# Kernel optimization log

Hardware: AMD Instinct MI355X
Metric: run time of the kernel (lower is better)

## Reference

```python
import jax, jax.numpy as jnp
import numpy as np

B, T, N, K, HD = 4, 32, 1024, 16, 128
IN_CH = 4


def _knn_idx(q, r, k):
    # q, r: [..., 3, N]. dist(n, m) = ||q[..., n] - r[..., m]||
    # expanded-norm form avoids materializing [..., 3, N, N]
    q2 = jnp.sum(q * q, axis=-2)                     # [..., N]
    r2 = jnp.sum(r * r, axis=-2)                     # [..., N]
    qr = jnp.einsum('...cn,...cm->...nm', q, r)      # [..., N, N]
    d2 = q2[..., :, None] + r2[..., None, :] - 2.0 * qr
    _, idx = jax.lax.top_k(-d2, k)                   # smallest-k (sqrt is monotone)
    return idx                                       # [..., N, K]


def _gather_nbrs(feat, idx):
    # feat [B, C, N], idx [B, N, K] -> [B, C, N, K]; out[b,c,n,k] = feat[b,c,idx[b,n,k]]
    return jax.vmap(lambda f, i: f[:, i])(feat, idx)


def _lstm_layer(cur_in, position, pos_past, group_ind, w, b, hd):
    # cur_in [B,T,C,N]; position/pos_past [B,T,4,N]; group_ind [B,T,N,K]
    Bb, Tt, C, Nn = cur_in.shape
    h0 = jnp.zeros((Bb, hd, Nn), cur_in.dtype)
    c0 = jnp.zeros_like(h0)

    def step(carry, inp):
        h, c = carry                                  # [B,hd,N]
        xt, pp, idx = inp                             # [B,C,N], [B,4,N], [B,N,K]
        h_with_pos = jnp.concatenate([pp, h], axis=1) # [B,4+hd,N]
        hg = _gather_nbrs(h_with_pos, idx)            # [B,4+hd,N,K]
        cg = _gather_nbrs(c, idx)                     # [B,hd,N,K]
        # cell subtracts center position from first 4 channels of hidden
        hg = jnp.concatenate([hg[:, :4] - xt[:, :4, :, None], hg[:, 4:]], axis=1)
        xk = jnp.broadcast_to(xt[..., None], xt.shape + (idx.shape[-1],))
        comb = jnp.concatenate([xk, hg], axis=1)      # [B, C+4+hd, N, K]
        gates = jnp.einsum('bink,oi->bonk', comb, w) + b[None, :, None, None]
        ci, cf, co, cgt = jnp.split(gates, 4, axis=1)
        c_next = jax.nn.sigmoid(cf) * cg + jax.nn.sigmoid(ci) * jnp.tanh(cgt)
        h_next = jax.nn.sigmoid(co) * jnp.tanh(c_next)
        h_new = jnp.max(h_next, axis=-1)              # AdaptiveMaxPool2d((None,1)) over K
        c_new = jnp.max(c_next, axis=-1)
        return (h_new, c_new), h_new

    xs = (jnp.moveaxis(cur_in, 1, 0), jnp.moveaxis(pos_past, 1, 0),
          jnp.moveaxis(group_ind, 1, 0))
    (h, c), hs = jax.lax.scan(step, (h0, c0), xs)
    hs = jnp.moveaxis(hs, 0, 1)                       # [B,T,hd,N]
    layer_out = jnp.concatenate([position, hs], axis=2)  # [B,T,4+hd,N]
    return layer_out, h, c


def _forward(x, w0, b0, w1, b1):
    position = x[:, :, :4]                            # [B,T,4,N]
    p3 = position[:, :, :3]
    idx0 = _knn_idx(p3[:, 0], p3[:, 0], K)[:, None]   # [B,1,N,K] (frame 0 vs itself)
    idxr = _knn_idx(p3[:, 1:], p3[:, :-1], K)         # [B,T-1,N,K] (frame t vs t-1)
    group_ind = jnp.concatenate([idx0, idxr], axis=1)  # [B,T,N,K]
    # past-frame positions (t=0 uses frame 0)
    pos_past = jnp.concatenate([position[:, :1], position[:, :-1]], axis=1)
    out0, h, c = _lstm_layer(x,    position, pos_past, group_ind, w0, b0, HD)
    out1, h, c = _lstm_layer(out0, position, pos_past, group_ind, w1, b1, HD)
    return out1, h, c, group_ind


def setup_inputs() -> dict:
    key = jax.random.key(0)
    ks = jax.random.split(key, 3)
    x = jax.random.normal(ks[0], (B, T, IN_CH, N), jnp.float32)
    # 1x1 conv weights flattened to [out, in]; layer0 in=4+4+128=136, layer1 in=132+4+128=264
    w0 = jax.random.normal(ks[1], (4 * HD, IN_CH + 4 + HD), jnp.float32) * 0.05
    b0 = jnp.zeros((4 * HD,), jnp.float32)
    w1 = jax.random.normal(ks[2], (4 * HD, (HD + 4) + 4 + HD), jnp.float32) * 0.05
    b1 = jnp.zeros((4 * HD,), jnp.float32)
    return {"x": x, "w0": w0, "b0": b0, "w1": w1, "b1": b1}


def reference(x, w0, b0, w1, b1):
    out1, h, c, group_ind = _forward(x, w0, b0, w1, b1)
    # match torch shapes: trailing singleton dim
    return out1[..., None], h[..., None], c[..., None], group_ind
```

## Files before the change

kernel.cpp:

```cpp
#include <hip/hip_runtime.h>
#include <math.h>

#define BB 4
#define TT 32
#define NN 1024
#define KK 16
#define HDIM 128
#define NO 512
#define KG 132

#define OUT1_SZ ((size_t)BB*TT*132*NN)
#define OH (OUT1_SZ)
#define OC (OH + (size_t)BB*HDIM*NN)
#define OG (OC + (size_t)BB*HDIM*NN)

__global__ __launch_bounds__(256) void prep_weights(
    const float* __restrict__ w0, const float* __restrict__ w1,
    float* __restrict__ WaT0, float* __restrict__ WgT0,
    float* __restrict__ WaT1, float* __restrict__ WgT1)
{
  int idx = blockIdx.x * 256 + threadIdx.x;
  if (idx >= KG * NO) return;
  int k = idx / NO, o = idx - k * NO;
  WgT0[idx] = w0[o * 136 + 4 + k];
  WgT1[idx] = w1[o * 264 + 132 + k];
  float a1 = w1[o * 264 + k];
  if (k < 4) a1 -= w1[o * 264 + 132 + k];
  WaT1[idx] = a1;
  if (k < 4) WaT0[k * NO + o] = w0[o * 136 + k] - w0[o * 136 + 4 + k];
}

__global__ __launch_bounds__(512) void knn_kernel(
    const float* __restrict__ x, int* __restrict__ gind, float* __restrict__ gfloat)
{
  __shared__ float rx[NN], ry[NN], rz[NN], rr[NN];
  int b = blockIdx.z, t = blockIdx.y;
  int tp = (t == 0) ? 0 : t - 1;
  const float* xr = x + (size_t)(b * TT + tp) * 4 * NN;
  for (int m = threadIdx.x; m < NN; m += 512) {
    float a = xr[m], e = xr[NN + m], c = xr[2 * NN + m];
    rx[m] = a; ry[m] = e; rz[m] = c;
    rr[m] = __fadd_rn(__fadd_rn(__fmul_rn(a, a), __fmul_rn(e, e)), __fmul_rn(c, c));
  }
  __syncthreads();
  int n = blockIdx.x * 512 + threadIdx.x;
  const float* xq = x + (size_t)(b * TT + t) * 4 * NN;
  float qx = xq[n], qy = xq[NN + n], qz = xq[2 * NN + n];
  float q2 = __fadd_rn(__fadd_rn(__fmul_rn(qx, qx), __fmul_rn(qy, qy)), __fmul_rn(qz, qz));
  float bd[KK]; int bi[KK];
#pragma unroll
  for (int i = 0; i < KK; ++i) { bd[i] = 3.402823466e38f; bi[i] = 0; }
  for (int m = 0; m < NN; ++m) {
    float s = __fmaf_rn(qz, rz[m], __fmaf_rn(qy, ry[m], __fmaf_rn(qx, rx[m], 0.0f)));
    float d2 = __fsub_rn(__fadd_rn(q2, rr[m]), __fmul_rn(2.0f, s));
    if (d2 < bd[KK - 1]) {
#pragma unroll
      for (int i = KK - 1; i > 0; --i) {
        float pv = bd[i - 1]; int pi = bi[i - 1];
        if (pv > d2)            { bd[i] = pv; bi[i] = pi; }
        else if (bd[i] > d2)    { bd[i] = d2; bi[i] = m; }
      }
      if (bd[0] > d2) { bd[0] = d2; bi[0] = m; }
    }
  }
  size_t base = ((size_t)(b * TT + t) * NN + n) * KK;
#pragma unroll
  for (int i = 0; i < KK; ++i) { gind[base + i] = bi[i]; gfloat[base + i] = (float)bi[i]; }
}

template<int KA>
__global__ __launch_bounds__(256) void gemm_ag(
    const float* __restrict__ WgT, const float* __restrict__ WaT,
    const float* __restrict__ bias, const float* __restrict__ x,
    const float* __restrict__ hTg, size_t hTg_bstr,
    const float* __restrict__ hTa,
    int t, int tp,
    float* __restrict__ Aout, float* __restrict__ Gout)
{
  int tid = threadIdx.x;
  int w = tid >> 6, lane = tid & 63;
  int o0u = __builtin_amdgcn_readfirstlane(blockIdx.y * 16 + w * 4);
  int n = blockIdx.x * 64 + lane;
  int b = blockIdx.z;

  float aG[4] = {0.f, 0.f, 0.f, 0.f};
  float aA[4] = {0.f, 0.f, 0.f, 0.f};

  const float* xg = x + (size_t)(b * TT + tp) * 4 * NN + n;
  const float* xa = x + (size_t)(b * TT + t) * 4 * NN + n;

#pragma unroll
  for (int k = 0; k < 4; ++k) {
    const float* wg = WgT + (size_t)k * NO + o0u;
    const float* wa = WaT + (size_t)k * NO + o0u;
    float gv = xg[(size_t)k * NN];
    float av = xa[(size_t)k * NN];
#pragma unroll
    for (int i = 0; i < 4; ++i) {
      aG[i] = fmaf(wg[i], gv, aG[i]);
      aA[i] = fmaf(wa[i], av, aA[i]);
    }
  }

  const float* hg = hTg + (size_t)b * hTg_bstr + n;
  const float* ha = hTa + (size_t)b * (HDIM * NN) + n;
#pragma unroll 4
  for (int k = 0; k < HDIM; ++k) {
    const float* wg = WgT + (size_t)(4 + k) * NO + o0u;
    float gv = hg[(size_t)k * NN];
#pragma unroll
    for (int i = 0; i < 4; ++i) aG[i] = fmaf(wg[i], gv, aG[i]);
    if (KA == 132) {
      const float* wa = WaT + (size_t)(4 + k) * NO + o0u;
      float av = ha[(size_t)k * NN];
#pragma unroll
      for (int i = 0; i < 4; ++i) aA[i] = fmaf(wa[i], av, aA[i]);
    }
  }

  const float* bv = bias + o0u;
  size_t row = ((size_t)b * NN + n) * NO + o0u;
  *(float4*)&Gout[row] = make_float4(aG[0], aG[1], aG[2], aG[3]);
  *(float4*)&Aout[row] = make_float4(aA[0] + bv[0], aA[1] + bv[1],
                                     aA[2] + bv[2], aA[3] + bv[3]);
}

__global__ __launch_bounds__(1024) void ew_step(
    const float* __restrict__ A, const float* __restrict__ G,
    const int* __restrict__ gind,
    const float* __restrict__ c_in, float* __restrict__ c_out,
    float* __restrict__ hT, size_t hT_bstr, int t)
{
  __shared__ float htile[HDIM][9];
  int tid = threadIdx.x;
  int j = tid & 127, ns = tid >> 7;
  int b = blockIdx.y;
  int n = blockIdx.x * 8 + ns;
  const float* Ap = A + ((size_t)b * NN + n) * NO;
  float a0 = Ap[j], a1 = Ap[128 + j], a2 = Ap[256 + j], a3 = Ap[384 + j];
  const int* ip = gind + ((size_t)(b * TT + t) * NN + n) * KK;
  const float* Gb = G + (size_t)b * NN * NO;
  const float* cb = c_in + (size_t)b * NN * HDIM;
  float hmax = -3.402823466e38f, cmax = -3.402823466e38f;
#pragma unroll 4
  for (int k = 0; k < KK; ++k) {
    int m = __builtin_amdgcn_readfirstlane(ip[k]);
    const float* Gp = Gb + (size_t)m * NO;
    float gi = a0 + Gp[j];
    float gf = a1 + Gp[128 + j];
    float go = a2 + Gp[256 + j];
    float gg = a3 + Gp[384 + j];
    float cg = cb[(size_t)m * HDIM + j];
    float si = 1.0f / (1.0f + __expf(-gi));
    float sf = 1.0f / (1.0f + __expf(-gf));
    float so = 1.0f / (1.0f + __expf(-go));
    float tg = 1.0f - 2.0f / (1.0f + __expf(2.0f * gg));
    float cn = sf * cg + si * tg;
    float tc = 1.0f - 2.0f / (1.0f + __expf(2.0f * cn));
    float hn = so * tc;
    hmax = fmaxf(hmax, hn);
    cmax = fmaxf(cmax, cn);
  }
  c_out[((size_t)b * NN + n) * HDIM + j] = cmax;
  htile[j][ns] = hmax;
  __syncthreads();
  int jw = tid >> 3, nn = tid & 7;
  hT[(size_t)b * hT_bstr + (size_t)jw * NN + blockIdx.x * 8 + nn] = htile[jw][nn];
}

__global__ __launch_bounds__(256) void transpose_nj_jn(
    const float* __restrict__ src, float* __restrict__ dst,
    size_t dstBase, size_t bStride)
{
  __shared__ float tl[64][65];
  int tid = threadIdx.x;
  int n0 = blockIdx.x * 64, j0 = blockIdx.y * 64, b = blockIdx.z;
  int c = tid & 63, r4 = tid >> 6;
#pragma unroll
  for (int i = 0; i < 16; ++i) {
    int r = r4 + i * 4;
    tl[r][c] = src[((size_t)b * NN + n0 + r) * HDIM + j0 + c];
  }
  __syncthreads();
  float* dp = dst + dstBase + (size_t)b * bStride;
#pragma unroll
  for (int i = 0; i < 16; ++i) {
    int rr = r4 + i * 4;
    dp[(size_t)(j0 + rr) * NN + n0 + c] = tl[c][rr];
  }
}

__global__ __launch_bounds__(256) void copy_h(const float* __restrict__ out1,
                                              float* __restrict__ dst)
{
  int i = blockIdx.x * 256 + threadIdx.x;
  if (i >= BB * HDIM * NN) return;
  int b = i / (HDIM * NN);
  int r = i - b * (HDIM * NN);
  dst[i] = out1[((size_t)(b * TT + TT - 1) * 132 + 4) * NN + r];
}

__global__ __launch_bounds__(256) void pos_copy(const float* __restrict__ x,
                                                float* __restrict__ out)
{
  int i = blockIdx.x * 256 + threadIdx.x;
  if (i >= BB * TT * 4 * NN) return;
  int n = i & (NN - 1);
  int btc = i >> 10;
  int c = btc & 3, bt = btc >> 2;
  out[((size_t)bt * 132 + c) * NN + n] = x[i];
}

extern "C" void kernel_launch(void* const* d_in, const int* in_sizes, int n_in,
                              void* d_out, int out_size, void* d_ws, size_t ws_size,
                              hipStream_t stream)
{
  const float* x  = (const float*)d_in[0];
  const float* w0 = (const float*)d_in[1];
  const float* b0 = (const float*)d_in[2];
  const float* w1 = (const float*)d_in[3];
  const float* b1 = (const float*)d_in[4];
  float* out = (float*)d_out;

  float* wsf = (float*)d_ws;
  int*   gind = (int*)d_ws;
  size_t off = (size_t)BB * TT * NN * KK;
  const size_t HSZ = (size_t)BB * NN * HDIM;
  float* h0T = wsf + off; off += HSZ;
  float* c0a = wsf + off; off += HSZ;
  float* c0b = wsf + off; off += HSZ;
  float* c1a = wsf + off; off += HSZ;
  float* c1b = wsf + off; off += HSZ;
  float* zeros = wsf + off; off += (size_t)HDIM * NN;
  float* Abuf = wsf + off; off += (size_t)BB * NN * NO;
  float* Gbuf = wsf + off; off += (size_t)BB * NN * NO;
  float* WaT0 = wsf + off; off += 4 * NO;
  float* WgT0 = wsf + off; off += (size_t)KG * NO;
  float* WaT1 = wsf + off; off += (size_t)KG * NO;
  float* WgT1 = wsf + off; off += (size_t)KG * NO;

  hipMemsetAsync(c0a, 0, HSZ * 4, stream);
  hipMemsetAsync(c1a, 0, HSZ * 4, stream);
  hipMemsetAsync(zeros, 0, (size_t)HDIM * NN * 4, stream);

  prep_weights<<<(KG * NO + 255) / 256, 256, 0, stream>>>(w0, w1, WaT0, WgT0, WaT1, WgT1);
  knn_kernel<<<dim3(2, TT, BB), 512, 0, stream>>>(x, gind, out + OG);
  pos_copy<<<(BB * TT * 4 * NN + 255) / 256, 256, 0, stream>>>(x, out);

  const size_t H_BSTR = (size_t)HDIM * NN;
  const size_t OUT_BSTR = (size_t)TT * 132 * NN;

  float* c0[2] = {c0a, c0b};
  float* c1[2] = {c1a, c1b};
  for (int t = 0; t < TT; ++t) {
    int tp = t ? t - 1 : 0;
    const float* hTg0 = t ? h0T : zeros;
    gemm_ag<4><<<dim3(16, 32, BB), 256, 0, stream>>>(
        WgT0, WaT0, b0, x, hTg0, t ? H_BSTR : 0, h0T, t, tp, Abuf, Gbuf);
    ew_step<<<dim3(NN / 8, BB), 1024, 0, stream>>>(
        Abuf, Gbuf, gind, c0[t & 1], c0[(t & 1) ^ 1], h0T, H_BSTR, t);
    const float* hTg1 = t ? (out + ((size_t)(t - 1) * 132 + 4) * NN) : zeros;
    gemm_ag<132><<<dim3(16, 32, BB), 256, 0, stream>>>(
        WgT1, WaT1, b1, x, hTg1, t ? OUT_BSTR : 0, h0T, t, tp, Abuf, Gbuf);
    ew_step<<<dim3(NN / 8, BB), 1024, 0, stream>>>(
        Abuf, Gbuf, gind, c1[t & 1], c1[(t & 1) ^ 1],
        out + ((size_t)t * 132 + 4) * NN, OUT_BSTR, t);
  }
  copy_h<<<(BB * HDIM * NN + 255) / 256, 256, 0, stream>>>(out, out + OH);
  transpose_nj_jn<<<dim3(16, 2, BB), 256, 0, stream>>>(c1[0], out, OC, (size_t)HDIM * NN);
}
```

Before: 3.938 ms.

## Merge both layers' gather GEMMs and fuse layer-1 center GEMM into layer-0 cell step

The per-timestep schedule drops from four launches to three. A single GEMM kernel now computes the neighbour-side projections for both layers, since those depend only on previous-step hidden states. The layer-1 center projection (the WaT1 x [pos, h0] product) moves into the layer-0 elementwise kernel, where it reads the new h0 tile from shared memory. This removes one launch, one global round trip of h0 for that GEMM, and a serial dependency, at the cost of a heavier elementwise kernel doing 128-term dot products per thread.

Result: slower. 4.706 ms (+19.5%).

```diff
diff --git a/kernel.cpp b/kernel.cpp
--- a/kernel.cpp
+++ b/kernel.cpp
@@ -68,14 +68,15 @@
   for (int i = 0; i < KK; ++i) { gind[base + i] = bi[i]; gfloat[base + i] = (float)bi[i]; }
 }
 
-template<int KA>
-__global__ __launch_bounds__(256) void gemm_ag(
-    const float* __restrict__ WgT, const float* __restrict__ WaT,
-    const float* __restrict__ bias, const float* __restrict__ x,
-    const float* __restrict__ hTg, size_t hTg_bstr,
-    const float* __restrict__ hTa,
+__global__ __launch_bounds__(256) void gemm_gg(
+    const float* __restrict__ WgT0, const float* __restrict__ WgT1,
+    const float* __restrict__ WaT0, const float* __restrict__ b0,
+    const float* __restrict__ x,
+    const float* __restrict__ h0T, size_t h0_bstr,
+    const float* __restrict__ h1T, size_t h1_bstr,
     int t, int tp,
-    float* __restrict__ Aout, float* __restrict__ Gout)
+    float* __restrict__ A0out, float* __restrict__ G0out,
+    float* __restrict__ G1out)
 {
   int tid = threadIdx.x;
   int w = tid >> 6, lane = tid & 63;
@@ -83,53 +84,59 @@
   int n = blockIdx.x * 64 + lane;
   int b = blockIdx.z;
 
-  float aG[4] = {0.f, 0.f, 0.f, 0.f};
-  float aA[4] = {0.f, 0.f, 0.f, 0.f};
+  float aG0[4] = {0.f, 0.f, 0.f, 0.f};
+  float aG1[4] = {0.f, 0.f, 0.f, 0.f};
+  float aA0[4] = {0.f, 0.f, 0.f, 0.f};
 
   const float* xg = x + (size_t)(b * TT + tp) * 4 * NN + n;
   const float* xa = x + (size_t)(b * TT + t) * 4 * NN + n;
 
 #pragma unroll
   for (int k = 0; k < 4; ++k) {
-    const float* wg = WgT + (size_t)k * NO + o0u;
-    const float* wa = WaT + (size_t)k * NO + o0u;
+    const float* wg0 = WgT0 + (size_t)k * NO + o0u;
+    const float* wg1 = WgT1 + (size_t)k * NO + o0u;
+    const float* wa0 = WaT0 + (size_t)k * NO + o0u;
     float gv = xg[(size_t)k * NN];
     float av = xa[(size_t)k * NN];
 #pragma unroll
     for (int i = 0; i < 4; ++i) {
-      aG[i] = fmaf(wg[i], gv, aG[i]);
-      aA[i] = fmaf(wa[i], av, aA[i]);
-    }
-  }
-
-  const float* hg = hTg + (size_t)b * hTg_bstr + n;
-  const float* ha = hTa + (size_t)b * (HDIM * NN) + n;
+      aG0[i] = fmaf(wg0[i], gv, aG0[i]);
+      aG1[i] = fmaf(wg1[i], gv, aG1[i]);
+      aA0[i] = fmaf(wa0[i], av, aA0[i]);
+    }
+  }
+
+  const float* h0 = h0T + (size_t)b * h0_bstr + n;
+  const float* h1 = h1T + (size_t)b * h1_bstr + n;
 #pragma unroll 4
   for (int k = 0; k < HDIM; ++k) {
-    const float* wg = WgT + (size_t)(4 + k) * NO + o0u;
-    float gv = hg[(size_t)k * NN];
-#pragma unroll
-    for (int i = 0; i < 4; ++i) aG[i] = fmaf(wg[i], gv, aG[i]);
-    if (KA == 132) {
-      const float* wa = WaT + (size_t)(4 + k) * NO + o0u;
-      float av = ha[(size_t)k * NN];
-#pragma unroll
-      for (int i = 0; i < 4; ++i) aA[i] = fmaf(wa[i], av, aA[i]);
-    }
-  }
-
-  const float* bv = bias + o0u;
+    const float* wg0 = WgT0 + (size_t)(4 + k) * NO + o0u;
+    const float* wg1 = WgT1 + (size_t)(4 + k) * NO + o0u;
+    float g0 = h0[(size_t)k * NN];
+    float g1 = h1[(size_t)k * NN];
+#pragma unroll
+    for (int i = 0; i < 4; ++i) {
+      aG0[i] = fmaf(wg0[i], g0, aG0[i]);
+      aG1[i] = fmaf(wg1[i], g1, aG1[i]);
+    }
+  }
+
+  const float* bv = b0 + o0u;
   size_t row = ((size_t)b * NN + n) * NO + o0u;
-  *(float4*)&Gout[row] = make_float4(aG[0], aG[1], aG[2], aG[3]);
-  *(float4*)&Aout[row] = make_float4(aA[0] + bv[0], aA[1] + bv[1],
-                                     aA[2] + bv[2], aA[3] + bv[3]);
-}
-
-__global__ __launch_bounds__(1024) void ew_step(
+  *(float4*)&G0out[row] = make_float4(aG0[0], aG0[1], aG0[2], aG0[3]);
+  *(float4*)&G1out[row] = make_float4(aG1[0], aG1[1], aG1[2], aG1[3]);
+  *(float4*)&A0out[row] = make_float4(aA0[0] + bv[0], aA0[1] + bv[1],
+                                      aA0[2] + bv[2], aA0[3] + bv[3]);
+}
+
+__global__ __launch_bounds__(1024) void ew0_a1(
     const float* __restrict__ A, const float* __restrict__ G,
     const int* __restrict__ gind,
     const float* __restrict__ c_in, float* __restrict__ c_out,
-    float* __restrict__ hT, size_t hT_bstr, int t)
+    float* __restrict__ hT, size_t hT_bstr,
+    const float* __restrict__ WaT1, const float* __restrict__ b1,
+    const float* __restrict__ x, int t,
+    float* __restrict__ A1out)
 {
   __shared__ float htile[HDIM][9];
   int tid = threadIdx.x;
@@ -164,6 +171,79 @@
   c_out[((size_t)b * NN + n) * HDIM + j] = cmax;
   htile[j][ns] = hmax;
   __syncthreads();
+  {
+    int jw = tid >> 3, nn = tid & 7;
+    hT[(size_t)b * hT_bstr + (size_t)jw * NN + blockIdx.x * 8 + nn] = htile[jw][nn];
+  }
+  {
+    int o4 = j * 4;
+    const float* xa = x + (size_t)(b * TT + t) * 4 * NN + n;
+    float p0 = xa[0], p1 = xa[NN], p2 = xa[2 * NN], p3 = xa[3 * NN];
+    float acc[4] = {0.f, 0.f, 0.f, 0.f};
+    {
+      float4 w0v = *(const float4*)&WaT1[0 * NO + o4];
+      float4 w1v = *(const float4*)&WaT1[1 * NO + o4];
+      float4 w2v = *(const float4*)&WaT1[2 * NO + o4];
+      float4 w3v = *(const float4*)&WaT1[3 * NO + o4];
+      acc[0] = fmaf(w0v.x, p0, fmaf(w1v.x, p1, fmaf(w2v.x, p2, fmaf(w3v.x, p3, acc[0]))));
+      acc[1] = fmaf(w0v.y, p0, fmaf(w1v.y, p1, fmaf(w2v.y, p2, fmaf(w3v.y, p3, acc[1]))));
+      acc[2] = fmaf(w0v.z, p0, fmaf(w1v.z, p1, fmaf(w2v.z, p2, fmaf(w3v.z, p3, acc[2]))));
+      acc[3] = fmaf(w0v.w, p0, fmaf(w1v.w, p1, fmaf(w2v.w, p2, fmaf(w3v.w, p3, acc[3]))));
+    }
+#pragma unroll 4
+    for (int k = 0; k < HDIM; ++k) {
+      float4 wv = *(const float4*)&WaT1[(size_t)(4 + k) * NO + o4];
+      float hv = htile[k][ns];
+      acc[0] = fmaf(wv.x, hv, acc[0]);
+      acc[1] = fmaf(wv.y, hv, acc[1]);
+      acc[2] = fmaf(wv.z, hv, acc[2]);
+      acc[3] = fmaf(wv.w, hv, acc[3]);
+    }
+    float4 bb = *(const float4*)&b1[o4];
+    *(float4*)&A1out[((size_t)b * NN + n) * NO + o4] =
+        make_float4(acc[0] + bb.x, acc[1] + bb.y, acc[2] + bb.z, acc[3] + bb.w);
+  }
+}
+
+__global__ __launch_bounds__(1024) void ew_step(
+    const float* __restrict__ A, const float* __restrict__ G,
+    const int* __restrict__ gind,
+    const float* __restrict__ c_in, float* __restrict__ c_out,
+    float* __restrict__ hT, size_t hT_bstr, int t)
+{
+  __shared__ float htile[HDIM][9];
+  int tid = threadIdx.x;
+  int j = tid & 127, ns = tid >> 7;
+  int b = blockIdx.y;
+  int n = blockIdx.x * 8 + ns;
+  const float* Ap = A + ((size_t)b * NN + n) * NO;
+  float a0 = Ap[j], a1 = Ap[128 + j], a2 = Ap[256 + j], a3 = Ap[384 + j];
+  const int* ip = gind + ((size_t)(b * TT + t) * NN + n) * KK;
+  const float* Gb = G + (size_t)b * NN * NO;
+  const float* cb = c_in + (size_t)b * NN * HDIM;
+  float hmax = -3.402823466e38f, cmax = -3.402823466e38f;
+#pragma unroll 4
+  for (int k = 0; k < KK; ++k) {
+    int m = __builtin_amdgcn_readfirstlane(ip[k]);
+    const float* Gp = Gb + (size_t)m * NO;
+    float gi = a0 + Gp[j];
+    float gf = a1 + Gp[128 + j];
+    float go = a2 + Gp[256 + j];
+    float gg = a3 + Gp[384 + j];
+    float cg = cb[(size_t)m * HDIM + j];
+    float si = 1.0f / (1.0f + __expf(-gi));
+    float sf = 1.0f / (1.0f + __expf(-gf));
+    float so = 1.0f / (1.0f + __expf(-go));
+    float tg = 1.0f - 2.0f / (1.0f + __expf(2.0f * gg));
+    float cn = sf * cg + si * tg;
+    float tc = 1.0f - 2.0f / (1.0f + __expf(2.0f * cn));
+    float hn = so * tc;
+    hmax = fmaxf(hmax, hn);
+    cmax = fmaxf(cmax, cn);
+  }
+  c_out[((size_t)b * NN + n) * HDIM + j] = cmax;
+  htile[j][ns] = hmax;
+  __syncthreads();
   int jw = tid >> 3, nn = tid & 7;
   hT[(size_t)b * hT_bstr + (size_t)jw * NN + blockIdx.x * 8 + nn] = htile[jw][nn];
 }
@@ -232,8 +312,10 @@
   float* c1a = wsf + off; off += HSZ;
   float* c1b = wsf + off; off += HSZ;
   float* zeros = wsf + off; off += (size_t)HDIM * NN;
-  float* Abuf = wsf + off; off += (size_t)BB * NN * NO;
-  float* Gbuf = wsf + off; off += (size_t)BB * NN * NO;
+  float* A0buf = wsf + off; off += (size_t)BB * NN * NO;
+  float* G0buf = wsf + off; off += (size_t)BB * NN * NO;
+  float* A1buf = wsf + off; off += (size_t)BB * NN * NO;
+  float* G1buf = wsf + off; off += (size_t)BB * NN * NO;
   float* WaT0 = wsf + off; off += 4 * NO;
   float* WgT0 = wsf + off; off += (size_t)KG * NO;
   float* WaT1 = wsf + off; off += (size_t)KG * NO;
@@ -254,16 +336,17 @@
   float* c1[2] = {c1a, c1b};
   for (int t = 0; t < TT; ++t) {
     int tp = t ? t - 1 : 0;
-    const float* hTg0 = t ? h0T : zeros;
-    gemm_ag<4><<<dim3(16, 32, BB), 256, 0, stream>>>(
-        WgT0, WaT0, b0, x, hTg0, t ? H_BSTR : 0, h0T, t, tp, Abuf, Gbuf);
+    const float* h0prev = t ? h0T : zeros;
+    const float* h1prev = t ? (out + ((size_t)(t - 1) * 132 + 4) * NN) : zeros;
+    gemm_gg<<<dim3(16, 32, BB), 256, 0, stream>>>(
+        WgT0, WgT1, WaT0, b0, x,
+        h0prev, t ? H_BSTR : 0, h1prev, t ? OUT_BSTR : 0,
+        t, tp, A0buf, G0buf, G1buf);
+    ew0_a1<<<dim3(NN / 8, BB), 1024, 0, stream>>>(
+        A0buf, G0buf, gind, c0[t & 1], c0[(t & 1) ^ 1], h0T, H_BSTR,
+        WaT1, b1, x, t, A1buf);
     ew_step<<<dim3(NN / 8, BB), 1024, 0, stream>>>(
-        Abuf, Gbuf, gind, c0[t & 1], c0[(t & 1) ^ 1], h0T, H_BSTR, t);
-    const float* hTg1 = t ? (out + ((size_t)(t - 1) * 132 + 4) * NN) : zeros;
-    gemm_ag<132><<<dim3(16, 32, BB), 256, 0, stream>>>(
-        WgT1, WaT1, b1, x, hTg1, t ? OUT_BSTR : 0, h0T, t, tp, Abuf, Gbuf);
-    ew_step<<<dim3(NN / 8, BB), 1024, 0, stream>>>(
-        Abuf, Gbuf, gind, c1[t & 1], c1[(t & 1) ^ 1],
+        A1buf, G1buf, gind, c1[t & 1], c1[(t & 1) ^ 1],
         out + ((size_t)t * 132 + 4) * NN, OUT_BSTR, t);
   }
   copy_h<<<(BB * HDIM * NN + 255) / 256, 256, 0, stream>>>(out, out + OH);
```

## Fuse the time-step loop into one persistent cooperative kernel with grid syncs

Applied to the files above, without the earlier changes.

Replaces the 128 per-step kernel launches with a single cooperative persistent kernel that loops over time and uses grid.sync between phases. The G-side GEMMs for both layers are merged into one phase because both depend only on the previous step's hidden states, which leaves four grid syncs per step. Separate A/G buffers are kept per layer. The aim is to remove launch overhead and serialization, at the cost of grid-sync latency and lower parallelism: 256 blocks of 1024 threads now share the work, and 1024-thread blocks with launch_bounds(1024,4) limit registers.

Measured after the change: 10.29 ms. 161% more time.

```diff
diff --git a/kernel.cpp b/kernel.cpp
--- a/kernel.cpp
+++ b/kernel.cpp
@@ -1,5 +1,8 @@
 #include <hip/hip_runtime.h>
+#include <hip/hip_cooperative_groups.h>
 #include <math.h>
+
+namespace cg = cooperative_groups;
 
 #define BB 4
 #define TT 32
@@ -68,104 +71,168 @@
   for (int i = 0; i < KK; ++i) { gind[base + i] = bi[i]; gfloat[base + i] = (float)bi[i]; }
 }
 
-template<int KA>
-__global__ __launch_bounds__(256) void gemm_ag(
-    const float* __restrict__ WgT, const float* __restrict__ WaT,
-    const float* __restrict__ bias, const float* __restrict__ x,
-    const float* __restrict__ hTg, size_t hTg_bstr,
-    const float* __restrict__ hTa,
-    int t, int tp,
-    float* __restrict__ Aout, float* __restrict__ Gout)
-{
-  int tid = threadIdx.x;
-  int w = tid >> 6, lane = tid & 63;
-  int o0u = __builtin_amdgcn_readfirstlane(blockIdx.y * 16 + w * 4);
-  int n = blockIdx.x * 64 + lane;
-  int b = blockIdx.z;
-
-  float aG[4] = {0.f, 0.f, 0.f, 0.f};
-  float aA[4] = {0.f, 0.f, 0.f, 0.f};
-
-  const float* xg = x + (size_t)(b * TT + tp) * 4 * NN + n;
-  const float* xa = x + (size_t)(b * TT + t) * 4 * NN + n;
-
-#pragma unroll
-  for (int k = 0; k < 4; ++k) {
-    const float* wg = WgT + (size_t)k * NO + o0u;
-    const float* wa = WaT + (size_t)k * NO + o0u;
-    float gv = xg[(size_t)k * NN];
-    float av = xa[(size_t)k * NN];
-#pragma unroll
-    for (int i = 0; i < 4; ++i) {
-      aG[i] = fmaf(wg[i], gv, aG[i]);
-      aA[i] = fmaf(wa[i], av, aA[i]);
-    }
-  }
-
-  const float* hg = hTg + (size_t)b * hTg_bstr + n;
-  const float* ha = hTa + (size_t)b * (HDIM * NN) + n;
-#pragma unroll 4
-  for (int k = 0; k < HDIM; ++k) {
-    const float* wg = WgT + (size_t)(4 + k) * NO + o0u;
-    float gv = hg[(size_t)k * NN];
-#pragma unroll
-    for (int i = 0; i < 4; ++i) aG[i] = fmaf(wg[i], gv, aG[i]);
-    if (KA == 132) {
-      const float* wa = WaT + (size_t)(4 + k) * NO + o0u;
-      float av = ha[(size_t)k * NN];
-#pragma unroll
-      for (int i = 0; i < 4; ++i) aA[i] = fmaf(wa[i], av, aA[i]);
-    }
-  }
-
-  const float* bv = bias + o0u;
-  size_t row = ((size_t)b * NN + n) * NO + o0u;
-  *(float4*)&Gout[row] = make_float4(aG[0], aG[1], aG[2], aG[3]);
-  *(float4*)&Aout[row] = make_float4(aA[0] + bv[0], aA[1] + bv[1],
-                                     aA[2] + bv[2], aA[3] + bv[3]);
-}
-
-__global__ __launch_bounds__(1024) void ew_step(
+struct LoopParams {
+  const float* x;
+  const int*   gind;
+  const float* WaT0; const float* WgT0; const float* WaT1; const float* WgT1;
+  const float* b0;   const float* b1;
+  float* h0T; const float* zeros;
+  float* c0a; float* c0b; float* c1a; float* c1b;
+  float* A0;  float* G0;  float* A1;  float* G1;
+  float* out;
+};
+
+__device__ __forceinline__ void ew_phase(
+    int bid, int nblk, int tid,
     const float* __restrict__ A, const float* __restrict__ G,
     const int* __restrict__ gind,
     const float* __restrict__ c_in, float* __restrict__ c_out,
-    float* __restrict__ hT, size_t hT_bstr, int t)
-{
+    float* __restrict__ hT, size_t hT_bstr, int t,
+    float (*htile)[9])
+{
+  int j = tid & 127, ns = tid >> 7;
+  for (int u = bid; u < 512; u += nblk) {
+    int b = u >> 7, nb8 = u & 127;
+    int n = nb8 * 8 + ns;
+    const float* Ap = A + ((size_t)b * NN + n) * NO;
+    float a0 = Ap[j], a1 = Ap[128 + j], a2 = Ap[256 + j], a3 = Ap[384 + j];
+    const int* ip = gind + ((size_t)(b * TT + t) * NN + n) * KK;
+    const float* Gb = G + (size_t)b * NN * NO;
+    const float* cb = c_in + (size_t)b * NN * HDIM;
+    float hmax = -3.402823466e38f, cmax = -3.402823466e38f;
+#pragma unroll 4
+    for (int k = 0; k < KK; ++k) {
+      int m = __builtin_amdgcn_readfirstlane(ip[k]);
+      const float* Gp = Gb + (size_t)m * NO;
+      float gi = a0 + Gp[j];
+      float gf = a1 + Gp[128 + j];
+      float go = a2 + Gp[256 + j];
+      float gg = a3 + Gp[384 + j];
+      float cg = cb[(size_t)m * HDIM + j];
+      float si = 1.0f / (1.0f + __expf(-gi));
+      float sf = 1.0f / (1.0f + __expf(-gf));
+      float so = 1.0f / (1.0f + __expf(-go));
+      float tg = 1.0f - 2.0f / (1.0f + __expf(2.0f * gg));
+      float cn = sf * cg + si * tg;
+      float tc = 1.0f - 2.0f / (1.0f + __expf(2.0f * cn));
+      float hn = so * tc;
+      hmax = fmaxf(hmax, hn);
+      cmax = fmaxf(cmax, cn);
+    }
+    c_out[((size_t)b * NN + n) * HDIM + j] = cmax;
+    htile[j][ns] = hmax;
+    __syncthreads();
+    int jw = tid >> 3, nn = tid & 7;
+    hT[(size_t)b * hT_bstr + (size_t)jw * NN + nb8 * 8 + nn] = htile[jw][nn];
+    __syncthreads();
+  }
+}
+
+__global__ __launch_bounds__(1024, 4) void lstm_loop(LoopParams p)
+{
+  cg::grid_group grid = cg::this_grid();
+  const int bid = blockIdx.x;
+  const int nblk = gridDim.x;
+  const int tid = threadIdx.x;
   __shared__ float htile[HDIM][9];
-  int tid = threadIdx.x;
-  int j = tid & 127, ns = tid >> 7;
-  int b = blockIdx.y;
-  int n = blockIdx.x * 8 + ns;
-  const float* Ap = A + ((size_t)b * NN + n) * NO;
-  float a0 = Ap[j], a1 = Ap[128 + j], a2 = Ap[256 + j], a3 = Ap[384 + j];
-  const int* ip = gind + ((size_t)(b * TT + t) * NN + n) * KK;
-  const float* Gb = G + (size_t)b * NN * NO;
-  const float* cb = c_in + (size_t)b * NN * HDIM;
-  float hmax = -3.402823466e38f, cmax = -3.402823466e38f;
+
+  const size_t H_BSTR = (size_t)HDIM * NN;
+  const size_t OUT_BSTR = (size_t)TT * 132 * NN;
+  const int w = tid >> 6, lane = tid & 63;
+
+  for (int t = 0; t < TT; ++t) {
+    int tp = t ? t - 1 : 0;
+    const float* h0prev = t ? p.h0T : p.zeros;
+    size_t h0bs = t ? H_BSTR : 0;
+    const float* h1prev = t ? (p.out + ((size_t)(t - 1) * 132 + 4) * NN) : p.zeros;
+    size_t h1bs = t ? OUT_BSTR : 0;
+    const float* c0in = (t & 1) ? p.c0b : p.c0a;
+    float*       c0out = (t & 1) ? p.c0a : p.c0b;
+    const float* c1in = (t & 1) ? p.c1b : p.c1a;
+    float*       c1out = (t & 1) ? p.c1a : p.c1b;
+
+    for (int u = bid; u < 512; u += nblk) {
+      int b = u >> 7, rest = u & 127, nb = rest >> 3, ob = rest & 7;
+      int o0u = __builtin_amdgcn_readfirstlane(ob * 64 + w * 4);
+      int n = nb * 64 + lane;
+      float aG0[4] = {0.f, 0.f, 0.f, 0.f};
+      float aG1[4] = {0.f, 0.f, 0.f, 0.f};
+      float aA0[4] = {0.f, 0.f, 0.f, 0.f};
+      const float* xg = p.x + (size_t)(b * TT + tp) * 4 * NN + n;
+      const float* xa = p.x + (size_t)(b * TT + t) * 4 * NN + n;
+#pragma unroll
+      for (int k = 0; k < 4; ++k) {
+        const float* wg0 = p.WgT0 + (size_t)k * NO + o0u;
+        const float* wg1 = p.WgT1 + (size_t)k * NO + o0u;
+        const float* wa0 = p.WaT0 + (size_t)k * NO + o0u;
+        float gv = xg[(size_t)k * NN];
+        float av = xa[(size_t)k * NN];
+#pragma unroll
+        for (int i = 0; i < 4; ++i) {
+          aG0[i] = fmaf(wg0[i], gv, aG0[i]);
+          aG1[i] = fmaf(wg1[i], gv, aG1[i]);
+          aA0[i] = fmaf(wa0[i], av, aA0[i]);
+        }
+      }
+      const float* h0 = h0prev + (size_t)b * h0bs + n;
+      const float* h1 = h1prev + (size_t)b * h1bs + n;
 #pragma unroll 4
-  for (int k = 0; k < KK; ++k) {
-    int m = __builtin_amdgcn_readfirstlane(ip[k]);
-    const float* Gp = Gb + (size_t)m * NO;
-    float gi = a0 + Gp[j];
-    float gf = a1 + Gp[128 + j];
-    float go = a2 + Gp[256 + j];
-    float gg = a3 + Gp[384 + j];
-    float cg = cb[(size_t)m * HDIM + j];
-    float si = 1.0f / (1.0f + __expf(-gi));
-    float sf = 1.0f / (1.0f + __expf(-gf));
-    float so = 1.0f / (1.0f + __expf(-go));
-    float tg = 1.0f - 2.0f / (1.0f + __expf(2.0f * gg));
-    float cn = sf * cg + si * tg;
-    float tc = 1.0f - 2.0f / (1.0f + __expf(2.0f * cn));
-    float hn = so * tc;
-    hmax = fmaxf(hmax, hn);
-    cmax = fmaxf(cmax, cn);
-  }
-  c_out[((size_t)b * NN + n) * HDIM + j] = cmax;
-  htile[j][ns] = hmax;
-  __syncthreads();
-  int jw = tid >> 3, nn = tid & 7;
-  hT[(size_t)b * hT_bstr + (size_t)jw * NN + blockIdx.x * 8 + nn] = htile[jw][nn];
+      for (int k = 0; k < HDIM; ++k) {
+        const float* wg0 = p.WgT0 + (size_t)(4 + k) * NO + o0u;
+        const float* wg1 = p.WgT1 + (size_t)(4 + k) * NO + o0u;
+        float g0 = h0[(size_t)k * NN];
+        float g1 = h1[(size_t)k * NN];
+#pragma unroll
+        for (int i = 0; i < 4; ++i) {
+          aG0[i] = fmaf(wg0[i], g0, aG0[i]);
+          aG1[i] = fmaf(wg1[i], g1, aG1[i]);
+        }
+      }
+      const float* bv = p.b0 + o0u;
+      size_t row = ((size_t)b * NN + n) * NO + o0u;
+      *(float4*)&p.G0[row] = make_float4(aG0[0], aG0[1], aG0[2], aG0[3]);
+      *(float4*)&p.G1[row] = make_float4(aG1[0], aG1[1], aG1[2], aG1[3]);
+      *(float4*)&p.A0[row] = make_float4(aA0[0] + bv[0], aA0[1] + bv[1],
+                                         aA0[2] + bv[2], aA0[3] + bv[3]);
+    }
+    grid.sync();
+
+    ew_phase(bid, nblk, tid, p.A0, p.G0, p.gind, c0in, c0out,
+             p.h0T, H_BSTR, t, htile);
+    grid.sync();
+
+    for (int u = bid; u < 512; u += nblk) {
+      int b = u >> 7, rest = u & 127, nb = rest >> 3, ob = rest & 7;
+      int o0u = __builtin_amdgcn_readfirstlane(ob * 64 + w * 4);
+      int n = nb * 64 + lane;
+      float aA[4] = {0.f, 0.f, 0.f, 0.f};
+      const float* xa = p.x + (size_t)(b * TT + t) * 4 * NN + n;
+#pragma unroll
+      for (int k = 0; k < 4; ++k) {
+        const float* wa = p.WaT1 + (size_t)k * NO + o0u;
+        float av = xa[(size_t)k * NN];
+#pragma unroll
+        for (int i = 0; i < 4; ++i) aA[i] = fmaf(wa[i], av, aA[i]);
+      }
+      const float* ha = p.h0T + (size_t)b * H_BSTR + n;
+#pragma unroll 4
+      for (int k = 0; k < HDIM; ++k) {
+        const float* wa = p.WaT1 + (size_t)(4 + k) * NO + o0u;
+        float av = ha[(size_t)k * NN];
+#pragma unroll
+        for (int i = 0; i < 4; ++i) aA[i] = fmaf(wa[i], av, aA[i]);
+      }
+      const float* bv = p.b1 + o0u;
+      size_t row = ((size_t)b * NN + n) * NO + o0u;
+      *(float4*)&p.A1[row] = make_float4(aA[0] + bv[0], aA[1] + bv[1],
+                                         aA[2] + bv[2], aA[3] + bv[3]);
+    }
+    grid.sync();
+
+    ew_phase(bid, nblk, tid, p.A1, p.G1, p.gind, c1in, c1out,
+             p.out + ((size_t)t * 132 + 4) * NN, OUT_BSTR, t, htile);
+    grid.sync();
+  }
 }
 
 __global__ __launch_bounds__(256) void transpose_nj_jn(
@@ -232,8 +299,10 @@
   float* c1a = wsf + off; off += HSZ;
   float* c1b = wsf + off; off += HSZ;
   float* zeros = wsf + off; off += (size_t)HDIM * NN;
-  float* Abuf = wsf + off; off += (size_t)BB * NN * NO;
-  float* Gbuf = wsf + off; off += (size_t)BB * NN * NO;
+  float* A0buf = wsf + off; off += (size_t)BB * NN * NO;
+  float* G0buf = wsf + off; off += (size_t)BB * NN * NO;
+  float* A1buf = wsf + off; off += (size_t)BB * NN * NO;
+  float* G1buf = wsf + off; off += (size_t)BB * NN * NO;
   float* WaT0 = wsf + off; off += 4 * NO;
   float* WgT0 = wsf + off; off += (size_t)KG * NO;
   float* WaT1 = wsf + off; off += (size_t)KG * NO;
@@ -247,25 +316,17 @@
   knn_kernel<<<dim3(2, TT, BB), 512, 0, stream>>>(x, gind, out + OG);
   pos_copy<<<(BB * TT * 4 * NN + 255) / 256, 256, 0, stream>>>(x, out);
 
-  const size_t H_BSTR = (size_t)HDIM * NN;
-  const size_t OUT_BSTR = (size_t)TT * 132 * NN;
-
-  float* c0[2] = {c0a, c0b};
-  float* c1[2] = {c1a, c1b};
-  for (int t = 0; t < TT; ++t) {
-    int tp = t ? t - 1 : 0;
-    const float* hTg0 = t ? h0T : zeros;
-    gemm_ag<4><<<dim3(16, 32, BB), 256, 0, stream>>>(
-        WgT0, WaT0, b0, x, hTg0, t ? H_BSTR : 0, h0T, t, tp, Abuf, Gbuf);
-    ew_step<<<dim3(NN / 8, BB), 1024, 0, stream>>>(
-        Abuf, Gbuf, gind, c0[t & 1], c0[(t & 1) ^ 1], h0T, H_BSTR, t);
-    const float* hTg1 = t ? (out + ((size_t)(t - 1) * 132 + 4) * NN) : zeros;
-    gemm_ag<132><<<dim3(16, 32, BB), 256, 0, stream>>>(
-        WgT1, WaT1, b1, x, hTg1, t ? OUT_BSTR : 0, h0T, t, tp, Abuf, Gbuf);
-    ew_step<<<dim3(NN / 8, BB), 1024, 0, stream>>>(
-        Abuf, Gbuf, gind, c1[t & 1], c1[(t & 1) ^ 1],
-        out + ((size_t)t * 132 + 4) * NN, OUT_BSTR, t);
-  }
+  LoopParams P;
+  P.x = x; P.gind = gind;
+  P.WaT0 = WaT0; P.WgT0 = WgT0; P.WaT1 = WaT1; P.WgT1 = WgT1;
+  P.b0 = b0; P.b1 = b1;
+  P.h0T = h0T; P.zeros = zeros;
+  P.c0a = c0a; P.c0b = c0b; P.c1a = c1a; P.c1b = c1b;
+  P.A0 = A0buf; P.G0 = G0buf; P.A1 = A1buf; P.G1 = G1buf;
+  P.out = out;
+  void* args[] = { &P };
+  hipLaunchCooperativeKernel((void*)lstm_loop, dim3(256), dim3(1024), args, 0, stream);
+
   copy_h<<<(BB * HDIM * NN + 255) / 256, 256, 0, stream>>>(out, out + OH);
-  transpose_nj_jn<<<dim3(16, 2, BB), 256, 0, stream>>>(c1[0], out, OC, (size_t)HDIM * NN);
-}
+  transpose_nj_jn<<<dim3(16, 2, BB), 256, 0, stream>>>(c1a, out, OC, (size_t)HDIM * NN);
+}
```
